# Kernel optimization log

Measured on AMD Instinct MI355X. Metric: run time of the kernel, lower is better.

Reference implementation:

```python
import jax, jax.numpy as jnp
import numpy as np


def _grid_pull_linear_zero(input, grid):
    """Trilinear grid_pull, bound='zero', extrapolate=False, prefilter=False.
    input: (B, C, Nx, Ny, Nz); grid: (B, 3, Xo, Yo, Zo) voxel coords.
    """
    g = jnp.moveaxis(grid, 1, -1)                      # (B, Xo, Yo, Zo, 3)
    B, C, Nx, Ny, Nz = input.shape
    sizes = jnp.array([Nx, Ny, Nz], dtype=jnp.int32)
    f = jnp.floor(g)
    w = g - f                                          # fractional part in [0,1)
    f = f.astype(jnp.int32)
    inp_flat = input.reshape(B, C, -1)                 # (B, C, Nx*Ny*Nz)
    out = jnp.zeros((B, C, g.shape[1] * g.shape[2] * g.shape[3]), input.dtype)
    for dx in (0, 1):
        for dy in (0, 1):
            for dz in (0, 1):
                off = jnp.array([dx, dy, dz], dtype=jnp.int32)
                idx = f + off                          # (B,Xo,Yo,Zo,3)
                # zero bound: out-of-range taps contribute nothing
                valid = jnp.all((idx >= 0) & (idx < sizes), axis=-1)
                wc = jnp.prod(jnp.where(off == 1, w, 1.0 - w), axis=-1)
                ic = jnp.clip(idx, 0, sizes - 1)
                flat = (ic[..., 0] * Ny + ic[..., 1]) * Nz + ic[..., 2]
                vals = jnp.take_along_axis(inp_flat, flat.reshape(B, 1, -1), axis=2)
                out = out + vals * (wc * valid).reshape(B, 1, -1).astype(input.dtype)
    out = out.reshape(B, C, g.shape[1], g.shape[2], g.shape[3])
    # extrapolate=False: zero voxels sampled outside the field of view
    inb = jnp.all((g >= 0) & (g <= (sizes - 1).astype(g.dtype)), axis=-1)
    return out * inb[:, None].astype(out.dtype)


def setup_inputs() -> dict:
    key = jax.random.key(0)
    k1, k2 = jax.random.split(key)
    B, C, N = 2, 2, 128
    input = jax.random.normal(k1, (B, C, N, N, N), dtype=jnp.float32)
    # voxel coordinates spanning the full input volume [0, N-1]
    grid = jax.random.uniform(k2, (B, 3, N, N, N), dtype=jnp.float32) * (N - 1)
    return {"input": input, "grid": grid}


def reference(input, grid):
    return _grid_pull_linear_zero(input, grid)
```

## Files before the change

### kernel.cpp

```cpp
#include <hip/hip_runtime.h>


#define NDIM 128
#define NV   (128 * 128 * 128)
#define NPTS (2 * NV)
#define NBINS 16
#define CAP  270336
#define NBLK 4096

typedef float f4 __attribute__((ext_vector_type(4)));
typedef float f2 __attribute__((ext_vector_type(2)));
typedef int   i4 __attribute__((ext_vector_type(4)));

__device__ __forceinline__ int bin_of(float x, int b) {
    int ix = (int)floorf(x);
    int slab = min(max(ix, 0), NDIM - 1) >> 4;
    return (b << 3) + slab;
}

__global__ void p0_zero(int* __restrict__ cursor) {
    if (threadIdx.x < 64) cursor[threadIdx.x] = 0;
}

__global__ __launch_bounds__(256) void p3_scatter(
    const float* __restrict__ grid,
    f4* __restrict__ rec,
    int* __restrict__ pos,
    int* __restrict__ cursor)
{
    __shared__ int lcnt[NBINS];
    __shared__ int lbase[NBINS];
    const int t  = blockIdx.x * blockDim.x + threadIdx.x;
    const int p4 = t << 2;
    const int b  = p4 >> 21;
    const int s  = p4 & (NV - 1);

    if (threadIdx.x < NBINS) lcnt[threadIdx.x] = 0;
    __syncthreads();

    const float* gbase = grid + (size_t)b * 3 * NV;
    const f4 gx = __builtin_nontemporal_load(reinterpret_cast<const f4*>(gbase + s));
    const f4 gy = __builtin_nontemporal_load(reinterpret_cast<const f4*>(gbase + NV + s));
    const f4 gz = __builtin_nontemporal_load(reinterpret_cast<const f4*>(gbase + 2 * NV + s));

    int mybin[4], myrank[4];
#pragma unroll
    for (int k = 0; k < 4; ++k) {
        mybin[k]  = bin_of(gx[k], b);
        myrank[k] = atomicAdd(&lcnt[mybin[k]], 1);
    }
    __syncthreads();
    if (threadIdx.x < NBINS)
        lbase[threadIdx.x] = atomicAdd(&cursor[threadIdx.x], lcnt[threadIdx.x]);
    __syncthreads();

    i4 dvec;
#pragma unroll
    for (int k = 0; k < 4; ++k) {
        const int d = mybin[k] * CAP + lbase[mybin[k]] + myrank[k];
        f4 r;
        r.x = gx[k]; r.y = gy[k]; r.z = gz[k];
        r.w = __int_as_float(p4 + k);
        __builtin_nontemporal_store(r, &rec[d]);
        dvec[k] = d;
    }
    __builtin_nontemporal_store(dvec, reinterpret_cast<i4*>(pos + p4));
}

__global__ __launch_bounds__(256) void p4_gather(
    const float* __restrict__ input,
    const f4* __restrict__ rec,
    f2* __restrict__ res,
    const int* __restrict__ cursor)
{
    const int bid = blockIdx.x;
    const int bin   = (bid < (NBLK / 2)) ? (bid & 7) : 8 + (bid & 7);
    const int chunk = (bid & (NBLK / 2 - 1)) >> 3;
    const int cnt   = cursor[bin];
    const int b     = bin >> 3;
    const int seg   = bin * CAP;
    const float* vin = input + (size_t)b * 2 * NV;

    for (int i = chunk * 1024 + (threadIdx.x << 2); i < cnt; i += 256 * 1024) {
#pragma unroll
        for (int k = 0; k < 4; ++k) {
            if (i + k >= cnt) break;
            const int d = seg + i + k;
            const f4 r = __builtin_nontemporal_load(&rec[d]);
            const float x = r.x, y = r.y, z = r.z;

            const float fx = floorf(x), fy = floorf(y), fz = floorf(z);
            const float wx = x - fx, wy = y - fy, wz = z - fz;
            const int ix = (int)fx, iy = (int)fy, iz = (int)fz;

            const bool inb = (x >= 0.0f) & (x <= (float)(NDIM - 1)) &
                             (y >= 0.0f) & (y <= (float)(NDIM - 1)) &
                             (z >= 0.0f) & (z <= (float)(NDIM - 1));
            const bool interior = inb &
                                  ((unsigned)ix < (unsigned)(NDIM - 1)) &
                                  ((unsigned)iy < (unsigned)(NDIM - 1)) &
                                  ((unsigned)iz < (unsigned)(NDIM - 1));
            float acc0 = 0.0f, acc1 = 0.0f;
            if (interior) {
                const int base = (ix << 14) + (iy << 7) + iz;
                const float wx0 = 1.0f - wx, wy0 = 1.0f - wy, wz0 = 1.0f - wz;
                const float w00 = wx0 * wy0, w01 = wx0 * wy;
                const float w10 = wx  * wy0, w11 = wx  * wy;
                const f2 a00 = *reinterpret_cast<const f2*>(vin + base);
                const f2 a01 = *reinterpret_cast<const f2*>(vin + base + 128);
                const f2 a10 = *reinterpret_cast<const f2*>(vin + base + 16384);
                const f2 a11 = *reinterpret_cast<const f2*>(vin + base + 16512);
                const f2 c00 = *reinterpret_cast<const f2*>(vin + NV + base);
                const f2 c01 = *reinterpret_cast<const f2*>(vin + NV + base + 128);
                const f2 c10 = *reinterpret_cast<const f2*>(vin + NV + base + 16384);
                const f2 c11 = *reinterpret_cast<const f2*>(vin + NV + base + 16512);
                const float z00 = fmaf(a00.y, wz, a00.x * wz0);
                const float z01 = fmaf(a01.y, wz, a01.x * wz0);
                const float z10 = fmaf(a10.y, wz, a10.x * wz0);
                const float z11 = fmaf(a11.y, wz, a11.x * wz0);
                acc0 = fmaf(z11, w11, fmaf(z10, w10, fmaf(z01, w01, z00 * w00)));
                const float u00 = fmaf(c00.y, wz, c00.x * wz0);
                const float u01 = fmaf(c01.y, wz, c01.x * wz0);
                const float u10 = fmaf(c10.y, wz, c10.x * wz0);
                const float u11 = fmaf(c11.y, wz, c11.x * wz0);
                acc1 = fmaf(u11, w11, fmaf(u10, w10, fmaf(u01, w01, u00 * w00)));
            } else if (inb) {
                for (int dx = 0; dx < 2; ++dx) {
                    const int X = ix + dx;
                    if ((unsigned)X >= (unsigned)NDIM) continue;
                    const float wxd = dx ? wx : 1.0f - wx;
                    for (int dy = 0; dy < 2; ++dy) {
                        const int Y = iy + dy;
                        if ((unsigned)Y >= (unsigned)NDIM) continue;
                        const float wyd = dy ? wy : 1.0f - wy;
                        for (int dz = 0; dz < 2; ++dz) {
                            const int Z = iz + dz;
                            if ((unsigned)Z >= (unsigned)NDIM) continue;
                            const float w = wxd * wyd * (dz ? wz : 1.0f - wz);
                            const int idx = (X << 14) + (Y << 7) + Z;
                            acc0 = fmaf(vin[idx], w, acc0);
                            acc1 = fmaf(vin[NV + idx], w, acc1);
                        }
                    }
                }
            }
            f2 o; o.x = acc0; o.y = acc1;
            res[d] = o;
        }
    }
}

__global__ __launch_bounds__(256) void p5_unpermute(
    const f2* __restrict__ res,
    const int* __restrict__ pos,
    float* __restrict__ out)
{
    const int t  = blockIdx.x * blockDim.x + threadIdx.x;
    const int p4 = t << 2;
    const int b  = p4 >> 21;
    const int s  = p4 & (NV - 1);

    const i4 dd = __builtin_nontemporal_load(reinterpret_cast<const i4*>(pos + p4));
    const f2 r0 = res[dd.x];
    const f2 r1 = res[dd.y];
    const f2 r2 = res[dd.z];
    const f2 r3 = res[dd.w];
    f4 o0, o1;
    o0.x = r0.x; o0.y = r1.x; o0.z = r2.x; o0.w = r3.x;
    o1.x = r0.y; o1.y = r1.y; o1.z = r2.y; o1.w = r3.y;
    float* obase = out + (size_t)b * 2 * NV + s;
    __builtin_nontemporal_store(o0, reinterpret_cast<f4*>(obase));
    __builtin_nontemporal_store(o1, reinterpret_cast<f4*>(obase + NV));
}

__global__ __launch_bounds__(256) void repack_kernel(
    const float* __restrict__ input, float* __restrict__ pk)
{
    const int t  = blockIdx.x * blockDim.x + threadIdx.x;
    const int v4 = t << 2;
    const int b  = v4 >> 21;
    const int v  = v4 & (NV - 1);
    const float* base = input + (size_t)b * 2 * NV;
    const f4 a = *reinterpret_cast<const f4*>(base + v);
    const f4 c = *reinterpret_cast<const f4*>(base + NV + v);
    f4 w0, w1;
    w0.x = a.x; w0.y = c.x; w0.z = a.y; w0.w = c.y;
    w1.x = a.z; w1.y = c.z; w1.z = a.w; w1.w = c.w;
    float* o = pk + (size_t)b * 2 * NV + 2 * v;
    *reinterpret_cast<f4*>(o)     = w0;
    *reinterpret_cast<f4*>(o + 4) = w1;
}

__global__ __launch_bounds__(256) void grid_pull_packed_kernel(
    const float* __restrict__ pk,
    const float* __restrict__ grid,
    float* __restrict__ out)
{
    const int t  = blockIdx.x * blockDim.x + threadIdx.x;
    const int p4 = t << 2;
    const int b  = p4 >> 21;
    const int s  = p4 & (NV - 1);
    const float* gbase = grid + (size_t)b * 3 * NV;
    const f4 gx = *reinterpret_cast<const f4*>(gbase + s);
    const f4 gy = *reinterpret_cast<const f4*>(gbase + NV + s);
    const f4 gz = *reinterpret_cast<const f4*>(gbase + 2 * NV + s);
    const float* p = pk + (size_t)b * 2 * NV;

    f4 o0, o1;
#pragma unroll
    for (int k = 0; k < 4; ++k) {
        const float x = gx[k], y = gy[k], z = gz[k];
        const float fx = floorf(x), fy = floorf(y), fz = floorf(z);
        const float wx = x - fx, wy = y - fy, wz = z - fz;
        const int ix = (int)fx, iy = (int)fy, iz = (int)fz;
        const bool inb = (x >= 0.0f) & (x <= (float)(NDIM - 1)) &
                         (y >= 0.0f) & (y <= (float)(NDIM - 1)) &
                         (z >= 0.0f) & (z <= (float)(NDIM - 1));
        float acc0 = 0.0f, acc1 = 0.0f;
        if (inb) {
            for (int dx = 0; dx < 2; ++dx) {
                const int X = ix + dx;
                if ((unsigned)X >= (unsigned)NDIM) continue;
                const float wxd = dx ? wx : 1.0f - wx;
                for (int dy = 0; dy < 2; ++dy) {
                    const int Y = iy + dy;
                    if ((unsigned)Y >= (unsigned)NDIM) continue;
                    const float wyd = dy ? wy : 1.0f - wy;
                    for (int dz = 0; dz < 2; ++dz) {
                        const int Z = iz + dz;
                        if ((unsigned)Z >= (unsigned)NDIM) continue;
                        const float w = wxd * wyd * (dz ? wz : 1.0f - wz);
                        const f2 v = *reinterpret_cast<const f2*>(
                            p + (X << 15) + (Y << 8) + (Z << 1));
                        acc0 = fmaf(v.x, w, acc0);
                        acc1 = fmaf(v.y, w, acc1);
                    }
                }
            }
        }
        o0[k] = acc0; o1[k] = acc1;
    }
    float* obase = out + (size_t)b * 2 * NV + s;
    *reinterpret_cast<f4*>(obase)      = o0;
    *reinterpret_cast<f4*>(obase + NV) = o1;
}

__global__ __launch_bounds__(256) void grid_pull_direct_kernel(
    const float* __restrict__ input,
    const float* __restrict__ grid,
    float* __restrict__ out)
{
    const int t  = blockIdx.x * blockDim.x + threadIdx.x;
    const int p4 = t << 2;
    const int b  = p4 >> 21;
    const int s  = p4 & (NV - 1);
    const float* gbase = grid + (size_t)b * 3 * NV;
    const f4 gx = *reinterpret_cast<const f4*>(gbase + s);
    const f4 gy = *reinterpret_cast<const f4*>(gbase + NV + s);
    const f4 gz = *reinterpret_cast<const f4*>(gbase + 2 * NV + s);
    const float* in0 = input + (size_t)b * 2 * NV;
    const float* in1 = in0 + NV;
    f4 o0, o1;
#pragma unroll
    for (int k = 0; k < 4; ++k) {
        const float x = gx[k], y = gy[k], z = gz[k];
        const float fx = floorf(x), fy = floorf(y), fz = floorf(z);
        const float wx = x - fx, wy = y - fy, wz = z - fz;
        const int ix = (int)fx, iy = (int)fy, iz = (int)fz;
        const bool inb = (x >= 0.0f) & (x <= (float)(NDIM - 1)) &
                         (y >= 0.0f) & (y <= (float)(NDIM - 1)) &
                         (z >= 0.0f) & (z <= (float)(NDIM - 1));
        float acc0 = 0.0f, acc1 = 0.0f;
        if (inb) {
            for (int dx = 0; dx < 2; ++dx) {
                const int X = ix + dx;
                if ((unsigned)X >= (unsigned)NDIM) continue;
                const float wxd = dx ? wx : 1.0f - wx;
                for (int dy = 0; dy < 2; ++dy) {
                    const int Y = iy + dy;
                    if ((unsigned)Y >= (unsigned)NDIM) continue;
                    const float wyd = dy ? wy : 1.0f - wy;
                    for (int dz = 0; dz < 2; ++dz) {
                        const int Z = iz + dz;
                        if ((unsigned)Z >= (unsigned)NDIM) continue;
                        const float w = wxd * wyd * (dz ? wz : 1.0f - wz);
                        const int idx = (X << 14) + (Y << 7) + Z;
                        acc0 = fmaf(in0[idx], w, acc0);
                        acc1 = fmaf(in1[idx], w, acc1);
                    }
                }
            }
        }
        o0[k] = acc0; o1[k] = acc1;
    }
    float* obase = out + (size_t)b * 2 * NV + s;
    *reinterpret_cast<f4*>(obase)      = o0;
    *reinterpret_cast<f4*>(obase + NV) = o1;
}

extern "C" void kernel_launch(void* const* d_in, const int* in_sizes, int n_in,
                              void* d_out, int out_size, void* d_ws, size_t ws_size,
                              hipStream_t stream) {
    const float* input = (const float*)d_in[0];
    const float* grid  = (const float*)d_in[1];
    float* out         = (float*)d_out;

    const size_t rec_bytes  = (size_t)NBINS * CAP * sizeof(f4);
    const size_t pos_bytes  = (size_t)NPTS * sizeof(int);
    const size_t res_bytes  = (size_t)NBINS * CAP * sizeof(f2);
    const size_t cur_bytes  = 256;
    const size_t need_bin   = rec_bytes + pos_bytes + res_bytes + cur_bytes;
    const size_t need_pack  = (size_t)2 * 2 * NV * sizeof(float);

    const int block = 256;

    if (ws_size >= need_bin) {
        char* w = (char*)d_ws;
        f4*  rec    = (f4*)w;
        int* pos    = (int*)(w + rec_bytes);
        f2*  res    = (f2*)(w + rec_bytes + pos_bytes);
        int* cursor = (int*)(w + rec_bytes + pos_bytes + res_bytes);

        p0_zero<<<1, 64, 0, stream>>>(cursor);
        p3_scatter<<<NBLK, block, 0, stream>>>(grid, rec, pos, cursor);
        p4_gather<<<NBLK, block, 0, stream>>>(input, rec, res, cursor);
        p5_unpermute<<<NBLK, block, 0, stream>>>(res, pos, out);
    } else if (ws_size >= need_pack) {
        float* pk = (float*)d_ws;
        repack_kernel<<<NBLK, block, 0, stream>>>(input, pk);
        grid_pull_packed_kernel<<<NBLK, block, 0, stream>>>(pk, grid, out);
    } else {
        grid_pull_direct_kernel<<<NBLK, block, 0, stream>>>(input, grid, out);
    }
}
```

Measured before the change: 343.1 us.

## Process batches sequentially with channel-interleaved repack and batched tap loads in binned gather

The binned path now runs per batch in a host loop and adds a repack kernel that interleaves the two channels. Each corner tap then needs one 16-byte load instead of two 8-byte loads from separate channel planes. The gather loop issues the rec loads and all tap loads for four points before doing any math, to raise memory-level parallelism. Per-batch processing shrinks the working set (the 16 MB packed volume plus the records) so it may stay in cache, at the cost of twice as many kernel launches and an extra repack pass over the input.

```diff
diff --git a/kernel.cpp b/kernel.cpp
--- a/kernel.cpp
+++ b/kernel.cpp
@@ -1,56 +1,64 @@
 #include <hip/hip_runtime.h>
 
 
-#define NDIM 128
-#define NV   (128 * 128 * 128)
-#define NPTS (2 * NV)
-#define NBINS 16
-#define CAP  270336
-#define NBLK 4096
+#define NDIM  128
+#define NV    (128 * 128 * 128)
+#define NPTS  (2 * NV)
+#define NSLAB 8
+#define CAP   270336
+#define NBLKB 2048
 
 typedef float f4 __attribute__((ext_vector_type(4)));
 typedef float f2 __attribute__((ext_vector_type(2)));
 typedef int   i4 __attribute__((ext_vector_type(4)));
 
-__device__ __forceinline__ int bin_of(float x, int b) {
-    int ix = (int)floorf(x);
-    int slab = min(max(ix, 0), NDIM - 1) >> 4;
-    return (b << 3) + slab;
-}
-
 __global__ void p0_zero(int* __restrict__ cursor) {
-    if (threadIdx.x < 64) cursor[threadIdx.x] = 0;
+    if (threadIdx.x < NSLAB) cursor[threadIdx.x] = 0;
+}
+
+__global__ __launch_bounds__(256) void p2_repack(
+    const float* __restrict__ inb,
+    float* __restrict__ pk)
+{
+    const int t  = blockIdx.x * blockDim.x + threadIdx.x;
+    const int v  = t << 2;
+    const f4 a = *reinterpret_cast<const f4*>(inb + v);
+    const f4 c = *reinterpret_cast<const f4*>(inb + NV + v);
+    f4 w0, w1;
+    w0.x = a.x; w0.y = c.x; w0.z = a.y; w0.w = c.y;
+    w1.x = a.z; w1.y = c.z; w1.z = a.w; w1.w = c.w;
+    float* o = pk + 2 * v;
+    *reinterpret_cast<f4*>(o)     = w0;
+    *reinterpret_cast<f4*>(o + 4) = w1;
 }
 
 __global__ __launch_bounds__(256) void p3_scatter(
-    const float* __restrict__ grid,
+    const float* __restrict__ gb,
     f4* __restrict__ rec,
     int* __restrict__ pos,
     int* __restrict__ cursor)
 {
-    __shared__ int lcnt[NBINS];
-    __shared__ int lbase[NBINS];
-    const int t  = blockIdx.x * blockDim.x + threadIdx.x;
-    const int p4 = t << 2;
-    const int b  = p4 >> 21;
-    const int s  = p4 & (NV - 1);
-
-    if (threadIdx.x < NBINS) lcnt[threadIdx.x] = 0;
+    __shared__ int lcnt[NSLAB];
+    __shared__ int lbase[NSLAB];
+    const int t = blockIdx.x * blockDim.x + threadIdx.x;
+    const int s = t << 2;
+
+    if (threadIdx.x < NSLAB) lcnt[threadIdx.x] = 0;
     __syncthreads();
 
-    const float* gbase = grid + (size_t)b * 3 * NV;
-    const f4 gx = __builtin_nontemporal_load(reinterpret_cast<const f4*>(gbase + s));
-    const f4 gy = __builtin_nontemporal_load(reinterpret_cast<const f4*>(gbase + NV + s));
-    const f4 gz = __builtin_nontemporal_load(reinterpret_cast<const f4*>(gbase + 2 * NV + s));
+    const f4 gx = __builtin_nontemporal_load(reinterpret_cast<const f4*>(gb + s));
+    const f4 gy = __builtin_nontemporal_load(reinterpret_cast<const f4*>(gb + NV + s));
+    const f4 gz = __builtin_nontemporal_load(reinterpret_cast<const f4*>(gb + 2 * NV + s));
 
     int mybin[4], myrank[4];
 #pragma unroll
     for (int k = 0; k < 4; ++k) {
-        mybin[k]  = bin_of(gx[k], b);
+        const int ix = (int)floorf(gx[k]);
+        mybin[k]  = min(max(ix, 0), NDIM - 1) >> 4;
         myrank[k] = atomicAdd(&lcnt[mybin[k]], 1);
     }
     __syncthreads();
-    if (threadIdx.x < NBINS)
+    if (threadIdx.x < NSLAB)
         lbase[threadIdx.x] = atomicAdd(&cursor[threadIdx.x], lcnt[threadIdx.x]);
     __syncthreads();
 
@@ -60,92 +68,100 @@
         const int d = mybin[k] * CAP + lbase[mybin[k]] + myrank[k];
         f4 r;
         r.x = gx[k]; r.y = gy[k]; r.z = gz[k];
-        r.w = __int_as_float(p4 + k);
+        r.w = __int_as_float(s + k);
         __builtin_nontemporal_store(r, &rec[d]);
         dvec[k] = d;
     }
-    __builtin_nontemporal_store(dvec, reinterpret_cast<i4*>(pos + p4));
+    __builtin_nontemporal_store(dvec, reinterpret_cast<i4*>(pos + s));
 }
 
 __global__ __launch_bounds__(256) void p4_gather(
-    const float* __restrict__ input,
+    const float* __restrict__ pk,
     const f4* __restrict__ rec,
     f2* __restrict__ res,
     const int* __restrict__ cursor)
 {
-    const int bid = blockIdx.x;
-    const int bin   = (bid < (NBLK / 2)) ? (bid & 7) : 8 + (bid & 7);
-    const int chunk = (bid & (NBLK / 2 - 1)) >> 3;
+    const int bin   = blockIdx.x & 7;
+    const int chunk = blockIdx.x >> 3;
     const int cnt   = cursor[bin];
-    const int b     = bin >> 3;
     const int seg   = bin * CAP;
-    const float* vin = input + (size_t)b * 2 * NV;
 
     for (int i = chunk * 1024 + (threadIdx.x << 2); i < cnt; i += 256 * 1024) {
+        bool live[4];
+        f4 r[4];
 #pragma unroll
         for (int k = 0; k < 4; ++k) {
-            if (i + k >= cnt) break;
-            const int d = seg + i + k;
-            const f4 r = __builtin_nontemporal_load(&rec[d]);
-            const float x = r.x, y = r.y, z = r.z;
-
+            live[k] = (i + k) < cnt;
+            r[k] = rec[live[k] ? (seg + i + k) : seg];
+        }
+        f4 t00[4], t01[4], t10[4], t11[4];
+        bool inb[4], interior[4];
+        float wx[4], wy[4], wz[4];
+        int ixa[4], iya[4], iza[4];
+#pragma unroll
+        for (int k = 0; k < 4; ++k) {
+            const float x = r[k].x, y = r[k].y, z = r[k].z;
             const float fx = floorf(x), fy = floorf(y), fz = floorf(z);
-            const float wx = x - fx, wy = y - fy, wz = z - fz;
+            wx[k] = x - fx; wy[k] = y - fy; wz[k] = z - fz;
             const int ix = (int)fx, iy = (int)fy, iz = (int)fz;
-
-            const bool inb = (x >= 0.0f) & (x <= (float)(NDIM - 1)) &
-                             (y >= 0.0f) & (y <= (float)(NDIM - 1)) &
-                             (z >= 0.0f) & (z <= (float)(NDIM - 1));
-            const bool interior = inb &
-                                  ((unsigned)ix < (unsigned)(NDIM - 1)) &
-                                  ((unsigned)iy < (unsigned)(NDIM - 1)) &
-                                  ((unsigned)iz < (unsigned)(NDIM - 1));
+            ixa[k] = ix; iya[k] = iy; iza[k] = iz;
+            inb[k] = (x >= 0.0f) & (x <= (float)(NDIM - 1)) &
+                     (y >= 0.0f) & (y <= (float)(NDIM - 1)) &
+                     (z >= 0.0f) & (z <= (float)(NDIM - 1));
+            interior[k] = inb[k] &
+                          ((unsigned)ix < (unsigned)(NDIM - 1)) &
+                          ((unsigned)iy < (unsigned)(NDIM - 1)) &
+                          ((unsigned)iz < (unsigned)(NDIM - 1));
+            const int base = interior[k] ? ((ix << 14) + (iy << 7) + iz) : 0;
+            const f4* q = reinterpret_cast<const f4*>(pk + 2 * base);
+            t00[k] = q[0];
+            t01[k] = q[64];
+            t10[k] = q[8192];
+            t11[k] = q[8256];
+        }
+#pragma unroll
+        for (int k = 0; k < 4; ++k) {
             float acc0 = 0.0f, acc1 = 0.0f;
-            if (interior) {
-                const int base = (ix << 14) + (iy << 7) + iz;
-                const float wx0 = 1.0f - wx, wy0 = 1.0f - wy, wz0 = 1.0f - wz;
-                const float w00 = wx0 * wy0, w01 = wx0 * wy;
-                const float w10 = wx  * wy0, w11 = wx  * wy;
-                const f2 a00 = *reinterpret_cast<const f2*>(vin + base);
-                const f2 a01 = *reinterpret_cast<const f2*>(vin + base + 128);
-                const f2 a10 = *reinterpret_cast<const f2*>(vin + base + 16384);
-                const f2 a11 = *reinterpret_cast<const f2*>(vin + base + 16512);
-                const f2 c00 = *reinterpret_cast<const f2*>(vin + NV + base);
-                const f2 c01 = *reinterpret_cast<const f2*>(vin + NV + base + 128);
-                const f2 c10 = *reinterpret_cast<const f2*>(vin + NV + base + 16384);
-                const f2 c11 = *reinterpret_cast<const f2*>(vin + NV + base + 16512);
-                const float z00 = fmaf(a00.y, wz, a00.x * wz0);
-                const float z01 = fmaf(a01.y, wz, a01.x * wz0);
-                const float z10 = fmaf(a10.y, wz, a10.x * wz0);
-                const float z11 = fmaf(a11.y, wz, a11.x * wz0);
-                acc0 = fmaf(z11, w11, fmaf(z10, w10, fmaf(z01, w01, z00 * w00)));
-                const float u00 = fmaf(c00.y, wz, c00.x * wz0);
-                const float u01 = fmaf(c01.y, wz, c01.x * wz0);
-                const float u10 = fmaf(c10.y, wz, c10.x * wz0);
-                const float u11 = fmaf(c11.y, wz, c11.x * wz0);
-                acc1 = fmaf(u11, w11, fmaf(u10, w10, fmaf(u01, w01, u00 * w00)));
-            } else if (inb) {
+            const float wz0 = 1.0f - wz[k];
+            if (interior[k]) {
+                const float wx0 = 1.0f - wx[k], wy0 = 1.0f - wy[k];
+                const float w00 = wx0 * wy0,  w01 = wx0 * wy[k];
+                const float w10 = wx[k] * wy0, w11 = wx[k] * wy[k];
+                const float z00a = fmaf(t00[k].z, wz[k], t00[k].x * wz0);
+                const float z01a = fmaf(t01[k].z, wz[k], t01[k].x * wz0);
+                const float z10a = fmaf(t10[k].z, wz[k], t10[k].x * wz0);
+                const float z11a = fmaf(t11[k].z, wz[k], t11[k].x * wz0);
+                acc0 = fmaf(z11a, w11, fmaf(z10a, w10, fmaf(z01a, w01, z00a * w00)));
+                const float z00b = fmaf(t00[k].w, wz[k], t00[k].y * wz0);
+                const float z01b = fmaf(t01[k].w, wz[k], t01[k].y * wz0);
+                const float z10b = fmaf(t10[k].w, wz[k], t10[k].y * wz0);
+                const float z11b = fmaf(t11[k].w, wz[k], t11[k].y * wz0);
+                acc1 = fmaf(z11b, w11, fmaf(z10b, w10, fmaf(z01b, w01, z00b * w00)));
+            } else if (inb[k]) {
                 for (int dx = 0; dx < 2; ++dx) {
-                    const int X = ix + dx;
+                    const int X = ixa[k] + dx;
                     if ((unsigned)X >= (unsigned)NDIM) continue;
-                    const float wxd = dx ? wx : 1.0f - wx;
+                    const float wxd = dx ? wx[k] : 1.0f - wx[k];
                     for (int dy = 0; dy < 2; ++dy) {
-                        const int Y = iy + dy;
+                        const int Y = iya[k] + dy;
                         if ((unsigned)Y >= (unsigned)NDIM) continue;
-                        const float wyd = dy ? wy : 1.0f - wy;
+                        const float wyd = dy ? wy[k] : 1.0f - wy[k];
                         for (int dz = 0; dz < 2; ++dz) {
-                            const int Z = iz + dz;
+                            const int Z = iza[k] + dz;
                             if ((unsigned)Z >= (unsigned)NDIM) continue;
-                            const float w = wxd * wyd * (dz ? wz : 1.0f - wz);
-                            const int idx = (X << 14) + (Y << 7) + Z;
-                            acc0 = fmaf(vin[idx], w, acc0);
-                            acc1 = fmaf(vin[NV + idx], w, acc1);
+                            const float w = wxd * wyd * (dz ? wz[k] : wz0);
+                            const f2 v = *reinterpret_cast<const f2*>(
+                                pk + 2 * ((X << 14) + (Y << 7) + Z));
+                            acc0 = fmaf(v.x, w, acc0);
+                            acc1 = fmaf(v.y, w, acc1);
                         }
                     }
                 }
             }
-            f2 o; o.x = acc0; o.y = acc1;
-            res[d] = o;
+            if (live[k]) {
+                f2 o; o.x = acc0; o.y = acc1;
+                res[seg + i + k] = o;
+            }
         }
     }
 }
@@ -153,14 +169,11 @@
 __global__ __launch_bounds__(256) void p5_unpermute(
     const f2* __restrict__ res,
     const int* __restrict__ pos,
-    float* __restrict__ out)
-{
-    const int t  = blockIdx.x * blockDim.x + threadIdx.x;
-    const int p4 = t << 2;
-    const int b  = p4 >> 21;
-    const int s  = p4 & (NV - 1);
-
-    const i4 dd = __builtin_nontemporal_load(reinterpret_cast<const i4*>(pos + p4));
+    float* __restrict__ outb)
+{
+    const int t = blockIdx.x * blockDim.x + threadIdx.x;
+    const int s = t << 2;
+    const i4 dd = __builtin_nontemporal_load(reinterpret_cast<const i4*>(pos + s));
     const f2 r0 = res[dd.x];
     const f2 r1 = res[dd.y];
     const f2 r2 = res[dd.z];
@@ -168,27 +181,8 @@
     f4 o0, o1;
     o0.x = r0.x; o0.y = r1.x; o0.z = r2.x; o0.w = r3.x;
     o1.x = r0.y; o1.y = r1.y; o1.z = r2.y; o1.w = r3.y;
-    float* obase = out + (size_t)b * 2 * NV + s;
-    __builtin_nontemporal_store(o0, reinterpret_cast<f4*>(obase));
-    __builtin_nontemporal_store(o1, reinterpret_cast<f4*>(obase + NV));
-}
-
-__global__ __launch_bounds__(256) void repack_kernel(
-    const float* __restrict__ input, float* __restrict__ pk)
-{
-    const int t  = blockIdx.x * blockDim.x + threadIdx.x;
-    const int v4 = t << 2;
-    const int b  = v4 >> 21;
-    const int v  = v4 & (NV - 1);
-    const float* base = input + (size_t)b * 2 * NV;
-    const f4 a = *reinterpret_cast<const f4*>(base + v);
-    const f4 c = *reinterpret_cast<const f4*>(base + NV + v);
-    f4 w0, w1;
-    w0.x = a.x; w0.y = c.x; w0.z = a.y; w0.w = c.y;
-    w1.x = a.z; w1.y = c.z; w1.z = a.w; w1.w = c.w;
-    float* o = pk + (size_t)b * 2 * NV + 2 * v;
-    *reinterpret_cast<f4*>(o)     = w0;
-    *reinterpret_cast<f4*>(o + 4) = w1;
+    __builtin_nontemporal_store(o0, reinterpret_cast<f4*>(outb + s));
+    __builtin_nontemporal_store(o1, reinterpret_cast<f4*>(outb + NV + s));
 }
 
 __global__ __launch_bounds__(256) void grid_pull_packed_kernel(
@@ -197,15 +191,14 @@
     float* __restrict__ out)
 {
     const int t  = blockIdx.x * blockDim.x + threadIdx.x;
-    const int p4 = t << 2;
-    const int b  = p4 >> 21;
-    const int s  = p4 & (NV - 1);
+    const int p4i = t << 2;
+    const int b  = p4i >> 21;
+    const int s  = p4i & (NV - 1);
     const float* gbase = grid + (size_t)b * 3 * NV;
     const f4 gx = *reinterpret_cast<const f4*>(gbase + s);
     const f4 gy = *reinterpret_cast<const f4*>(gbase + NV + s);
     const f4 gz = *reinterpret_cast<const f4*>(gbase + 2 * NV + s);
     const float* p = pk + (size_t)b * 2 * NV;
-
     f4 o0, o1;
 #pragma unroll
     for (int k = 0; k < 4; ++k) {
@@ -251,9 +244,9 @@
     float* __restrict__ out)
 {
     const int t  = blockIdx.x * blockDim.x + threadIdx.x;
-    const int p4 = t << 2;
-    const int b  = p4 >> 21;
-    const int s  = p4 & (NV - 1);
+    const int p4i = t << 2;
+    const int b  = p4i >> 21;
+    const int s  = p4i & (NV - 1);
     const float* gbase = grid + (size_t)b * 3 * NV;
     const f4 gx = *reinterpret_cast<const f4*>(gbase + s);
     const f4 gy = *reinterpret_cast<const f4*>(gbase + NV + s);
@@ -305,31 +298,40 @@
     const float* grid  = (const float*)d_in[1];
     float* out         = (float*)d_out;
 
-    const size_t rec_bytes  = (size_t)NBINS * CAP * sizeof(f4);
-    const size_t pos_bytes  = (size_t)NPTS * sizeof(int);
-    const size_t res_bytes  = (size_t)NBINS * CAP * sizeof(f2);
-    const size_t cur_bytes  = 256;
-    const size_t need_bin   = rec_bytes + pos_bytes + res_bytes + cur_bytes;
-    const size_t need_pack  = (size_t)2 * 2 * NV * sizeof(float);
+    const size_t rec_bytes = (size_t)NSLAB * CAP * sizeof(f4);
+    const size_t res_bytes = (size_t)NSLAB * CAP * sizeof(f2);
+    const size_t pk_bytes  = (size_t)2 * NV * sizeof(float);
+    const size_t pos_bytes = (size_t)NV * sizeof(int);
+    const size_t need_bin  = rec_bytes + res_bytes + pk_bytes + pos_bytes + 256;
+    const size_t need_pack = (size_t)2 * 2 * NV * sizeof(float);
 
     const int block = 256;
 
     if (ws_size >= need_bin) {
         char* w = (char*)d_ws;
-        f4*  rec    = (f4*)w;
-        int* pos    = (int*)(w + rec_bytes);
-        f2*  res    = (f2*)(w + rec_bytes + pos_bytes);
-        int* cursor = (int*)(w + rec_bytes + pos_bytes + res_bytes);
-
-        p0_zero<<<1, 64, 0, stream>>>(cursor);
-        p3_scatter<<<NBLK, block, 0, stream>>>(grid, rec, pos, cursor);
-        p4_gather<<<NBLK, block, 0, stream>>>(input, rec, res, cursor);
-        p5_unpermute<<<NBLK, block, 0, stream>>>(res, pos, out);
+        f4*   rec    = (f4*)w;
+        f2*   res    = (f2*)(w + rec_bytes);
+        float* pk    = (float*)(w + rec_bytes + res_bytes);
+        int*  pos    = (int*)(w + rec_bytes + res_bytes + pk_bytes);
+        int*  cursor = (int*)(w + rec_bytes + res_bytes + pk_bytes + pos_bytes);
+
+        for (int b = 0; b < 2; ++b) {
+            const float* inb = input + (size_t)b * 2 * NV;
+            const float* gb  = grid  + (size_t)b * 3 * NV;
+            float* outb      = out   + (size_t)b * 2 * NV;
+            p0_zero<<<1, 64, 0, stream>>>(cursor);
+            p2_repack<<<NBLKB, block, 0, stream>>>(inb, pk);
+            p3_scatter<<<NBLKB, block, 0, stream>>>(gb, rec, pos, cursor);
+            p4_gather<<<NBLKB, block, 0, stream>>>(pk, rec, res, cursor);
+            p5_unpermute<<<NBLKB, block, 0, stream>>>(res, pos, outb);
+        }
     } else if (ws_size >= need_pack) {
         float* pk = (float*)d_ws;
-        repack_kernel<<<NBLK, block, 0, stream>>>(input, pk);
-        grid_pull_packed_kernel<<<NBLK, block, 0, stream>>>(pk, grid, out);
+        for (int b = 0; b < 2; ++b)
+            p2_repack<<<NBLKB, block, 0, stream>>>(input + (size_t)b * 2 * NV,
+                                                   pk + (size_t)b * 2 * NV);
+        grid_pull_packed_kernel<<<2 * NBLKB, block, 0, stream>>>(pk, grid, out);
     } else {
-        grid_pull_direct_kernel<<<NBLK, block, 0, stream>>>(input, grid, out);
-    }
-}
+        grid_pull_direct_kernel<<<2 * NBLKB, block, 0, stream>>>(input, grid, out);
+    }
+}
```

Result: faster. 298.4 us (-13.0%).
